# Kernel optimization log

Hardware: AMD Instinct MI355X
Metric: run time of the kernel (lower is better)

## Reference

```python
import jax, jax.numpy as jnp
import numpy as np
from functools import partial

# geometry: [W1, W2, H1, H2, L1, L2] -> x range, y range, z range
GEOM = (-16.0, 16.0, -16.0, 16.0, -16.0, 16.0)
T_MEAN = jnp.array([-0.25, 0.01, 0.26, 0.46, 0.26, 0.62, 0.69, 1.46], jnp.float32)
T_STD = jnp.array([0.93, 0.26, 0.53, 0.89, 1.11, 0.13, 0.16, 0.19], jnp.float32)
M_CAND = 1024   # cap on candidates passing cls > 0.5 (top-k by score)
IOU_THR = 0.5
CLS_THR = 0.5
# 8 corner sign combos for (x, y, z)
SIGNS = jnp.array([[sx, sy, sz] for sx in (1.0, -1.0) for sy in (1.0, -1.0) for sz in (1.0, -1.0)], jnp.float32)


def _pairwise_iou(b):
    # b: [M, 4] in (min0, min1, max0, max1)
    area = jnp.clip(b[:, 2] - b[:, 0], 0) * jnp.clip(b[:, 3] - b[:, 1], 0)
    lt = jnp.maximum(b[:, None, :2], b[None, :, :2])
    rb = jnp.minimum(b[:, None, 2:], b[None, :, 2:])
    wh = jnp.clip(rb - lt, 0)
    inter = wh[..., 0] * wh[..., 1]
    union = area[:, None] + area[None, :] - inter
    return inter / jnp.maximum(union, 1e-9)


def _nms_keep(boxes, valid, thr):
    # boxes already sorted by descending score; greedy NMS like torchvision ops.nms
    M = boxes.shape[0]
    iou = _pairwise_iou(boxes)
    ar = jnp.arange(M)

    def body(i, st):
        keep, sup = st
        k = valid[i] & jnp.logical_not(sup[i])
        keep = keep.at[i].set(k)
        sup = sup | (k & (iou[i] > thr) & (ar > i))
        return keep, sup

    keep, _ = jax.lax.fori_loop(0, M, body, (jnp.zeros(M, bool), jnp.zeros(M, bool)))
    return keep


def _decode(points):
    B, C, Z, Y, X = points.shape
    x0, x1, y0, y1, z0, z1 = GEOM
    xs = x0 + (x1 - x0) / X * jnp.arange(X, dtype=jnp.float32)
    ys = y0 + (y1 - y0) / Y * jnp.arange(Y, dtype=jnp.float32)
    zs = z0 + (z1 - z0) / Z * jnp.arange(Z, dtype=jnp.float32)
    zz, yy, xx = jnp.meshgrid(zs, ys, xs, indexing='ij')  # [Z,Y,X]
    cls = points[:, 0]  # [B,Z,Y,X], untouched by normalization
    reg = points[:, 1:9] * T_STD[None, :, None, None, None] + T_MEAN[None, :, None, None, None]
    cos_t, sin_t, dx, dy, dz, log_w, log_h, log_l = [reg[:, i] for i in range(8)]
    theta = jnp.arctan2(sin_t, cos_t)
    cx = xx[None] + dx
    cy = yy[None] + dy
    cz = zz[None] + dz
    w, h, l = jnp.exp(log_w), jnp.exp(log_h), jnp.exp(log_l)
    return cls, cx, cy, cz, w, h, l, theta


def _per_batch(cls, cx, cy, cz, w, h, l, theta, n_out):
    sc, idx = jax.lax.top_k(cls.reshape(-1), M_CAND)
    valid = sc > CLS_THR
    g = lambda a: a.reshape(-1)[idx]
    cxf, cyf, czf, wf, hf, lf, thf = g(cx), g(cy), g(cz), g(w), g(h), g(l), g(theta)
    zeros = jnp.zeros_like(thf)
    box9 = jnp.stack([cxf, cyf, czf, wf, hf, lf, zeros, thf, zeros], axis=-1)  # [M,9]
    # corners: half-size offsets rotated by Ry(theta) (rx = rz = 0)
    off = 0.5 * SIGNS[None, :, :] * jnp.stack([wf, hf, lf], -1)[:, None, :]  # [M,8,3]
    ct, st = jnp.cos(thf)[:, None], jnp.sin(thf)[:, None]
    ox, oy, oz = off[..., 0], off[..., 1], off[..., 2]
    px = cxf[:, None] + ct * ox + st * oz
    py = cyf[:, None] + oy
    pz = czf[:, None] - st * ox + ct * oz
    xmin, xmax = px.min(-1), px.max(-1)
    ymin, ymax = py.min(-1), py.max(-1)
    zmin, zmax = pz.min(-1), pz.max(-1)
    xy_box = jnp.stack([xmin, ymin, xmax, ymax], -1)
    yz_box = jnp.stack([ymin, zmin, ymax, zmax], -1)
    keep = _nms_keep(xy_box, valid, IOU_THR) | _nms_keep(yz_box, valid, IOU_THR)
    # compact kept boxes to the front (score order), pad with zeros to n_out
    order = jnp.argsort(jnp.where(keep, 0, 1))[:n_out]  # stable sort
    kv = keep[order]
    boxes_out = box9[order] * kv[:, None].astype(box9.dtype)
    scores_out = sc[order] * kv.astype(sc.dtype)
    return boxes_out, scores_out


def setup_inputs() -> dict:
    key = jax.random.key(0)
    B, Z, Y, X = 4, 64, 128, 128
    points = jax.random.normal(key, (B, 9, Z, Y, X), dtype=jnp.float32)
    points = points.at[:, 0].add(-3.0)
    return {"points": points, "label_shape": 0, "n_out": 50}


def reference(points, label_shape, n_out):
    cls, cx, cy, cz, w, h, l, theta = _decode(points)
    boxes, scores = jax.vmap(partial(_per_batch, n_out=n_out))(cls, cx, cy, cz, w, h, l, theta)
    return boxes, scores  # [B, n_out, 9], [B, n_out]
```

## Files before the change

kernel.cpp:

```cpp
#include <hip/hip_runtime.h>

typedef unsigned long long u64;

#define ZYX (64 * 128 * 128)
#define CAP 2048
#define VMAX 1024
#define MMAX 1024
#define MFAST 320
#define NCH 5
#define NTH 1024
#define NWAVE (NTH / 64)
#define CLS_THR 0.5f
#define IOU_THR 0.5f

__constant__ const float TM[8] = {-0.25f, 0.01f, 0.26f, 0.46f, 0.26f, 0.62f, 0.69f, 1.46f};
__constant__ const float TS[8] = {0.93f, 0.26f, 0.53f, 0.89f, 1.11f, 0.13f, 0.16f, 0.19f};

__device__ __forceinline__ void decode_from_r(const float* r, int f,
                                              float& cx, float& cy, float& cz,
                                              float& w, float& h, float& l, float& th) {
    int z = f >> 14;
    int y = (f >> 7) & 127;
    int x = f & 127;
    th = atan2f(r[1], r[0]);
    cx = (-16.0f + 0.25f * (float)x) + r[2];
    cy = (-16.0f + 0.25f * (float)y) + r[3];
    cz = (-16.0f + 0.5f * (float)z) + r[4];
    w = expf(r[5]);
    h = expf(r[6]);
    l = expf(r[7]);
}

__device__ __forceinline__ void decode_one(const float* __restrict__ pb, int f,
                                           float& cx, float& cy, float& cz,
                                           float& w, float& h, float& l, float& th) {
    float r[8];
#pragma unroll
    for (int c = 0; c < 8; ++c)
        r[c] = pb[(size_t)(c + 1) * ZYX + f] * TS[c] + TM[c];
    decode_from_r(r, f, cx, cy, cz, w, h, l, th);
}

__device__ __forceinline__ void corner_boxes(float cx, float cy, float cz,
                                             float w, float h, float l, float th,
                                             float& xmn, float& ymn, float& xmx, float& ymx,
                                             float& zmn, float& zmx) {
    float ct = cosf(th), st = sinf(th);
    xmn = 1e30f; xmx = -1e30f; ymn = 1e30f; ymx = -1e30f; zmn = 1e30f; zmx = -1e30f;
#pragma unroll
    for (int k = 0; k < 8; ++k) {
        float sx = (k & 4) ? -1.0f : 1.0f;
        float sy = (k & 2) ? -1.0f : 1.0f;
        float sz = (k & 1) ? -1.0f : 1.0f;
        float ox = 0.5f * sx * w;
        float oy = 0.5f * sy * h;
        float oz = 0.5f * sz * l;
        float px = cx + ct * ox + st * oz;
        float py = cy + oy;
        float pz = cz - st * ox + ct * oz;
        xmn = fminf(xmn, px); xmx = fmaxf(xmx, px);
        ymn = fminf(ymn, py); ymx = fmaxf(ymx, py);
        zmn = fminf(zmn, pz); zmx = fmaxf(zmx, pz);
    }
}

__device__ __forceinline__ bool iou_over(float ax0, float ay0, float ax1, float ay1, float aarea,
                                         float bx0, float by0, float bx1, float by1, float barea) {
    float lt0 = fmaxf(ax0, bx0), lt1 = fmaxf(ay0, by0);
    float rb0 = fminf(ax1, bx1), rb1 = fminf(ay1, by1);
    float inter = fmaxf(rb0 - lt0, 0.0f) * fmaxf(rb1 - lt1, 0.0f);
    float uni = aarea + barea - inter;
    return inter / fmaxf(uni, 1e-9f) > IOU_THR;
}

__global__ __launch_bounds__(256) void collect_kernel(const float* __restrict__ points, int B,
                                                      int* __restrict__ cnt,
                                                      float* __restrict__ csc,
                                                      int* __restrict__ cidx) {
    int g = blockIdx.x * blockDim.x + threadIdx.x;
    int per_b4 = ZYX / 4;
    int total4 = B * per_b4;
    if (g >= total4) return;
    int b = g / per_b4;
    int f4 = g - b * per_b4;
    const float4* p = (const float4*)(points + (size_t)b * 9 * ZYX);
    float4 v = p[f4];
    float vals[4] = {v.x, v.y, v.z, v.w};
    int f = f4 * 4;
#pragma unroll
    for (int k = 0; k < 4; ++k) {
        if (vals[k] > CLS_THR) {
            int pos = atomicAdd(&cnt[b], 1);
            if (pos < CAP) {
                csc[b * CAP + pos] = vals[k];
                cidx[b * CAP + pos] = f + k;
            }
        }
    }
}

__global__ __launch_bounds__(NTH, 1) void nms_kernel(const float* __restrict__ points,
                                                     const int* __restrict__ cnt,
                                                     const float* __restrict__ csc,
                                                     const int* __restrict__ cidx,
                                                     float4* __restrict__ wbxy,
                                                     float4* __restrict__ wbyz,
                                                     float2* __restrict__ war,
                                                     float* __restrict__ out,
                                                     int B, int n_out) {
    __shared__ float s_sc[VMAX];
    __shared__ int s_ix[VMAX];
    __shared__ int s_r2o[MMAX];
    __shared__ float s_reg[MFAST * 8];
    __shared__ float4 s_bxy[MFAST];
    __shared__ float4 s_byz[MFAST];
    __shared__ float2 s_ar[MFAST];
    __shared__ u64 s_colx[MFAST * NCH];
    __shared__ u64 s_coly[MFAST * NCH];
    __shared__ u64 s_keptw[16];

    int b = blockIdx.x;
    int tid = threadIdx.x;
    const float* pb = points + (size_t)b * 9 * ZYX;

    int V = cnt[b];
    if (V > VMAX) V = VMAX;
    for (int i = tid; i < V; i += NTH) {
        s_sc[i] = csc[b * CAP + i];
        s_ix[i] = cidx[b * CAP + i];
    }
    __syncthreads();

    int M = V < MMAX ? V : MMAX;
    int nchw = (M + 63) >> 6;
    bool fast = (M <= MFAST);

    for (int i = tid; i < V; i += NTH) {
        float si = s_sc[i];
        int ii = s_ix[i];
        int r = 0;
        for (int j = 0; j < V; ++j) {
            float sj = s_sc[j];
            int ij = s_ix[j];
            bool before = (sj > si) || (sj == si && ij < ii);
            r += before ? 1 : 0;
        }
        if (r < MMAX) s_r2o[r] = i;
    }
    __syncthreads();

    if (fast) {
        int M8 = M * 8;
        for (int t = tid; t < M8; t += NTH) {
            int m = t >> 3, c = t & 7;
            int f = s_ix[s_r2o[m]];
            s_reg[t] = pb[(size_t)(c + 1) * ZYX + f] * TS[c] + TM[c];
        }
        __syncthreads();
        for (int m = tid; m < M; m += NTH) {
            float r[8];
#pragma unroll
            for (int c = 0; c < 8; ++c) r[c] = s_reg[m * 8 + c];
            int f = s_ix[s_r2o[m]];
            float cx, cy, cz, w, h, l, th;
            decode_from_r(r, f, cx, cy, cz, w, h, l, th);
            float xmn, ymn, xmx, ymx, zmn, zmx;
            corner_boxes(cx, cy, cz, w, h, l, th, xmn, ymn, xmx, ymx, zmn, zmx);
            s_bxy[m] = make_float4(xmn, ymn, xmx, ymx);
            s_byz[m] = make_float4(ymn, zmn, ymx, zmx);
            float axy = fmaxf(xmx - xmn, 0.0f) * fmaxf(ymx - ymn, 0.0f);
            float ayz = fmaxf(ymx - ymn, 0.0f) * fmaxf(zmx - zmn, 0.0f);
            s_ar[m] = make_float2(axy, ayz);
        }
        __syncthreads();

        int wid = tid >> 6, lane = tid & 63;
        for (int j = wid; j < M; j += NWAVE) {
            float4 jxy = s_bxy[j], jyz = s_byz[j];
            float2 ja = s_ar[j];
            int smax = j >> 6;
            for (int s = 0; s <= smax; ++s) {
                int i = (s << 6) | lane;
                float4 ixy = s_bxy[i];
                float2 ia = s_ar[i];
                bool p = (i < j);
                bool ax = p && iou_over(ixy.x, ixy.y, ixy.z, ixy.w, ia.x,
                                        jxy.x, jxy.y, jxy.z, jxy.w, ja.x);
                u64 wxw = __ballot(ax);
                float4 iyz = s_byz[i];
                bool ay = p && iou_over(iyz.x, iyz.y, iyz.z, iyz.w, ia.y,
                                        jyz.x, jyz.y, jyz.z, jyz.w, ja.y);
                u64 wyw = __ballot(ay);
                if (lane == 0) {
                    s_colx[j * NCH + s] = wxw;
                    s_coly[j * NCH + s] = wyw;
                }
            }
        }
        __syncthreads();

        if (tid < 64) {
            int lane = tid;
            u64 extx = 0, exty = 0;
            for (int s = 0; s < nchw; ++s) {
                int c = s * 64 + lane;
                bool have = c < M;
                u64 wx = have ? s_colx[c * NCH + s] : 0ull;
                u64 wy = have ? s_coly[c * NCH + s] : 0ull;
                bool ex = (extx >> s) & 1ull;
                bool ey = (exty >> s) & 1ull;
                bool sup = ex;
                for (;;) {
                    u64 K = __ballot(!sup && have);
                    bool ns = ex | ((wx & K) != 0ull);
                    u64 ch = __ballot(ns != sup);
                    sup = ns;
                    if (!ch) break;
                }
                u64 Kx = __ballot(!sup && have);
                bool supy = ey;
                for (;;) {
                    u64 K = __ballot(!supy && have);
                    bool ns = ey | ((wy & K) != 0ull);
                    u64 ch = __ballot(ns != supy);
                    supy = ns;
                    if (!ch) break;
                }
                u64 Ky = __ballot(!supy && have);
                if (lane == 0) s_keptw[s] = Kx | Ky;
                for (int s2 = s + 1; s2 < nchw; ++s2) {
                    int c2 = s2 * 64 + lane;
                    if (c2 < M) {
                        if (s_colx[c2 * NCH + s] & Kx) extx |= 1ull << s2;
                        if (s_coly[c2 * NCH + s] & Ky) exty |= 1ull << s2;
                    }
                }
            }
        }
    } else {
        for (int r = tid; r < M; r += NTH) {
            float cx, cy, cz, w, h, l, th;
            decode_one(pb, s_ix[s_r2o[r]], cx, cy, cz, w, h, l, th);
            float xmn, ymn, xmx, ymx, zmn, zmx;
            corner_boxes(cx, cy, cz, w, h, l, th, xmn, ymn, xmx, ymx, zmn, zmx);
            wbxy[b * MMAX + r] = make_float4(xmn, ymn, xmx, ymx);
            wbyz[b * MMAX + r] = make_float4(ymn, zmn, ymx, zmx);
            float axy = fmaxf(xmx - xmn, 0.0f) * fmaxf(ymx - ymn, 0.0f);
            float ayz = fmaxf(ymx - ymn, 0.0f) * fmaxf(zmx - zmn, 0.0f);
            war[b * MMAX + r] = make_float2(axy, ayz);
        }
        __syncthreads();
        if (tid == 0) {
            char* supx = (char*)s_colx;
            char* supy = ((char*)s_colx) + MMAX;
            for (int s = 0; s < 16; ++s) s_keptw[s] = 0ull;
            for (int i = 0; i < M; ++i) { supx[i] = 0; supy[i] = 0; }
            int nk = 0;
            for (int i = 0; i < M; ++i) {
                bool kx = !supx[i], ky = !supy[i];
                if (!(kx | ky)) continue;
                s_keptw[i >> 6] |= 1ull << (i & 63);
                if (++nk >= n_out) break;
                float4 ixy = wbxy[b * MMAX + i], iyz = wbyz[b * MMAX + i];
                float2 ia = war[b * MMAX + i];
                for (int j = i + 1; j < M; ++j) {
                    float4 jxy = wbxy[b * MMAX + j];
                    float2 ja = war[b * MMAX + j];
                    if (kx && !supx[j] &&
                        iou_over(ixy.x, ixy.y, ixy.z, ixy.w, ia.x,
                                 jxy.x, jxy.y, jxy.z, jxy.w, ja.x)) supx[j] = 1;
                    float4 jyz = wbyz[b * MMAX + j];
                    if (ky && !supy[j] &&
                        iou_over(iyz.x, iyz.y, iyz.z, iyz.w, ia.y,
                                 jyz.x, jyz.y, jyz.z, jyz.w, ja.y)) supy[j] = 1;
                }
            }
        }
    }
    __syncthreads();

    float* boxes_out = out;
    float* scores_out = out + (size_t)B * n_out * 9;
    for (int p = tid; p < n_out; p += NTH) {
        int m = -1, total = 0;
        for (int s = 0; s < nchw; ++s) {
            u64 w = s_keptw[s];
            int pc = __popcll(w);
            if (m < 0 && p < total + pc) {
                int need = p - total;
                for (int q = 0; q < need; ++q) w &= w - 1ull;
                int bit = __ffsll((long long)w) - 1;
                m = s * 64 + bit;
            }
            total += pc;
        }
        float o9[9] = {0, 0, 0, 0, 0, 0, 0, 0, 0};
        float sc = 0.0f;
        if (m >= 0) {
            int o = s_r2o[m];
            int f = s_ix[o];
            float cx, cy, cz, w, h, l, th;
            if (fast) {
                float r[8];
#pragma unroll
                for (int c = 0; c < 8; ++c) r[c] = s_reg[m * 8 + c];
                decode_from_r(r, f, cx, cy, cz, w, h, l, th);
            } else {
                decode_one(pb, f, cx, cy, cz, w, h, l, th);
            }
            o9[0] = cx; o9[1] = cy; o9[2] = cz;
            o9[3] = w;  o9[4] = h;  o9[5] = l;
            o9[6] = 0.0f; o9[7] = th; o9[8] = 0.0f;
            sc = s_sc[o];
        }
        float* bo = boxes_out + ((size_t)b * n_out + p) * 9;
#pragma unroll
        for (int k = 0; k < 9; ++k) bo[k] = o9[k];
        scores_out[(size_t)b * n_out + p] = sc;
    }
}

extern "C" void kernel_launch(void* const* d_in, const int* in_sizes, int n_in,
                              void* d_out, int out_size, void* d_ws, size_t ws_size,
                              hipStream_t stream) {
    const float* points = (const float*)d_in[0];
    int B = in_sizes[0] / (9 * ZYX);
    int n_out = out_size / (B * 10);

    char* ws = (char*)d_ws;
    size_t off = 0;
    int* cnt = (int*)(ws + off); off += 256;
    float* csc = (float*)(ws + off); off += (size_t)B * CAP * 4;
    int* cidx = (int*)(ws + off); off += (size_t)B * CAP * 4;
    float4* wbxy = (float4*)(ws + off); off += (size_t)B * MMAX * 16;
    float4* wbyz = (float4*)(ws + off); off += (size_t)B * MMAX * 16;
    float2* war = (float2*)(ws + off); off += (size_t)B * MMAX * 8;

    hipMemsetAsync(cnt, 0, 256, stream);

    int total4 = B * (ZYX / 4);
    collect_kernel<<<(total4 + 255) / 256, 256, 0, stream>>>(points, B, cnt, csc, cidx);
    nms_kernel<<<B, NTH, 0, stream>>>(points, cnt, csc, cidx, wbxy, wbyz, war,
                                      (float*)d_out, B, n_out);
}
```

Baseline: 229.8 us.

## Collect candidates per-block in shared memory and drop global atomics and memset

Each collect block now scans a fixed segment of the cls channel with a grid-stride loop and appends hits through shared-memory atomics into 64 local slots, then writes its count and slots to global memory. The NMS kernel builds a prefix sum over the per-block counts and gathers candidates in order. This removes the hipMemsetAsync launch and contention on one global atomic counter per batch, and cuts the collect grid from many small blocks to 512 larger ones. In exchange, the NMS kernel does a serial prefix scan, and candidates are silently dropped if a segment has more than 64 hits.

New measurement: 224.1 us. 2.5% less time.

```diff
diff --git a/kernel.cpp b/kernel.cpp
--- a/kernel.cpp
+++ b/kernel.cpp
@@ -3,7 +3,9 @@
 typedef unsigned long long u64;
 
 #define ZYX (64 * 128 * 128)
-#define CAP 2048
+#define CPB 128
+#define SEG (ZYX / CPB)
+#define SLOTS 64
 #define VMAX 1024
 #define MMAX 1024
 #define MFAST 320
@@ -73,36 +75,48 @@
     return inter / fmaxf(uni, 1e-9f) > IOU_THR;
 }
 
-__global__ __launch_bounds__(256) void collect_kernel(const float* __restrict__ points, int B,
-                                                      int* __restrict__ cnt,
-                                                      float* __restrict__ csc,
-                                                      int* __restrict__ cidx) {
-    int g = blockIdx.x * blockDim.x + threadIdx.x;
-    int per_b4 = ZYX / 4;
-    int total4 = B * per_b4;
-    if (g >= total4) return;
-    int b = g / per_b4;
-    int f4 = g - b * per_b4;
-    const float4* p = (const float4*)(points + (size_t)b * 9 * ZYX);
-    float4 v = p[f4];
-    float vals[4] = {v.x, v.y, v.z, v.w};
-    int f = f4 * 4;
-#pragma unroll
-    for (int k = 0; k < 4; ++k) {
-        if (vals[k] > CLS_THR) {
-            int pos = atomicAdd(&cnt[b], 1);
-            if (pos < CAP) {
-                csc[b * CAP + pos] = vals[k];
-                cidx[b * CAP + pos] = f + k;
-            }
-        }
+__global__ __launch_bounds__(256) void collect_kernel(const float* __restrict__ points,
+                                                      int* __restrict__ gcnt,
+                                                      float* __restrict__ gsc,
+                                                      int* __restrict__ gix) {
+    __shared__ float s_ssc[SLOTS];
+    __shared__ int s_six[SLOTS];
+    __shared__ int s_n;
+    int g = blockIdx.x;
+    int b = g >> 7;
+    int c = g & (CPB - 1);
+    int tid = threadIdx.x;
+    if (tid == 0) s_n = 0;
+    __syncthreads();
+    const float4* p4 = (const float4*)(points + (size_t)b * 9 * ZYX) + (size_t)c * (SEG / 4);
+    int base = c * SEG;
+#pragma unroll
+    for (int k = 0; k < SEG / 4 / 256; ++k) {
+        int t4 = k * 256 + tid;
+        float4 v = p4[t4];
+        float vals[4] = {v.x, v.y, v.z, v.w};
+        int f = base + t4 * 4;
+#pragma unroll
+        for (int q = 0; q < 4; ++q) {
+            if (vals[q] > CLS_THR) {
+                int s = atomicAdd(&s_n, 1);
+                if (s < SLOTS) { s_ssc[s] = vals[q]; s_six[s] = f + q; }
+            }
+        }
+    }
+    __syncthreads();
+    int n = s_n < SLOTS ? s_n : SLOTS;
+    if (tid == 0) gcnt[g] = n;
+    for (int i = tid; i < n; i += 256) {
+        gsc[g * SLOTS + i] = s_ssc[i];
+        gix[g * SLOTS + i] = s_six[i];
     }
 }
 
 __global__ __launch_bounds__(NTH, 1) void nms_kernel(const float* __restrict__ points,
-                                                     const int* __restrict__ cnt,
-                                                     const float* __restrict__ csc,
-                                                     const int* __restrict__ cidx,
+                                                     const int* __restrict__ gcnt,
+                                                     const float* __restrict__ gsc,
+                                                     const int* __restrict__ gix,
                                                      float4* __restrict__ wbxy,
                                                      float4* __restrict__ wbyz,
                                                      float2* __restrict__ war,
@@ -118,16 +132,28 @@
     __shared__ u64 s_colx[MFAST * NCH];
     __shared__ u64 s_coly[MFAST * NCH];
     __shared__ u64 s_keptw[16];
+    __shared__ int s_cnt[CPB], s_pre[CPB];
 
     int b = blockIdx.x;
     int tid = threadIdx.x;
     const float* pb = points + (size_t)b * 9 * ZYX;
 
-    int V = cnt[b];
+    if (tid < CPB) s_cnt[tid] = gcnt[b * CPB + tid];
+    __syncthreads();
+    if (tid < CPB) {
+        int pre = 0;
+        for (int i = 0; i < CPB; ++i) { int v = s_cnt[i]; if (i < tid) pre += v; }
+        s_pre[tid] = pre;
+    }
+    __syncthreads();
+    int V = s_pre[CPB - 1] + s_cnt[CPB - 1];
     if (V > VMAX) V = VMAX;
-    for (int i = tid; i < V; i += NTH) {
-        s_sc[i] = csc[b * CAP + i];
-        s_ix[i] = cidx[b * CAP + i];
+    if (tid < CPB) {
+        int n = s_cnt[tid], o = s_pre[tid], g = b * CPB + tid;
+        for (int i = 0; i < n; ++i) {
+            int d = o + i;
+            if (d < VMAX) { s_sc[d] = gsc[g * SLOTS + i]; s_ix[d] = gix[g * SLOTS + i]; }
+        }
     }
     __syncthreads();
 
@@ -329,17 +355,14 @@
 
     char* ws = (char*)d_ws;
     size_t off = 0;
-    int* cnt = (int*)(ws + off); off += 256;
-    float* csc = (float*)(ws + off); off += (size_t)B * CAP * 4;
-    int* cidx = (int*)(ws + off); off += (size_t)B * CAP * 4;
+    int* gcnt = (int*)(ws + off); off += (size_t)B * CPB * sizeof(int); off = (off + 255) & ~(size_t)255;
+    float* gsc = (float*)(ws + off); off += (size_t)B * CPB * SLOTS * 4;
+    int* gix = (int*)(ws + off); off += (size_t)B * CPB * SLOTS * 4;
     float4* wbxy = (float4*)(ws + off); off += (size_t)B * MMAX * 16;
     float4* wbyz = (float4*)(ws + off); off += (size_t)B * MMAX * 16;
     float2* war = (float2*)(ws + off); off += (size_t)B * MMAX * 8;
 
-    hipMemsetAsync(cnt, 0, 256, stream);
-
-    int total4 = B * (ZYX / 4);
-    collect_kernel<<<(total4 + 255) / 256, 256, 0, stream>>>(points, B, cnt, csc, cidx);
-    nms_kernel<<<B, NTH, 0, stream>>>(points, cnt, csc, cidx, wbxy, wbyz, war,
+    collect_kernel<<<B * CPB, 256, 0, stream>>>(points, gcnt, gsc, gix);
+    nms_kernel<<<B, NTH, 0, stream>>>(points, gcnt, gsc, gix, wbxy, wbyz, war,
                                       (float*)d_out, B, n_out);
 }
```
